# Kernel optimization log

Measured on AMD Instinct MI355X. Metric: run time of the kernel, lower is better.

Reference implementation:

```python
import jax, jax.numpy as jnp
import numpy as np

BN_EPS = 1e-5
K = 3  # k_size


def _unfold(x, k):
    # torch F.unfold with padding=k//2, stride=1, viewed as (B, C, k*k, H, W).
    # Kernel positions are row-major (i slow, j fast), matching torch layout.
    p = k // 2
    B, C, H, W = x.shape
    xp = jnp.pad(x, ((0, 0), (0, 0), (p, p), (p, p)))
    pats = jnp.stack([xp[:, :, i:i + H, j:j + W]
                      for i in range(k) for j in range(k)], axis=2)
    return pats  # (B, C, k*k, H, W)


def _conv1x1(x, w, b):
    # w: (C_out, C_in), x: (B, C_in, H, W)
    return jnp.einsum('oc,bchw->bohw', w, x) + b[None, :, None, None]


def _bn(x, gamma, beta, mean, var):
    inv = gamma / jnp.sqrt(var + BN_EPS)
    return x * inv[None, :, None, None] + (beta - mean * inv)[None, :, None, None]


def setup_inputs() -> dict:
    key = jax.random.key(0)
    ks = jax.random.split(key, 12)
    B, C, H, W = 8, 256, 64, 64
    s = lambda k_, *sh: jax.random.normal(k_, sh, dtype=jnp.float32) * 0.05
    return {
        'x': jax.random.normal(ks[0], (B, C, H, W), dtype=jnp.float32),
        # feature_embedding: Conv2d(C, C, 1) + BN
        'w_embed': s(ks[1], C, C), 'b_embed': jnp.zeros((C,), jnp.float32),
        'bn1_gamma': jnp.ones((C,), jnp.float32), 'bn1_beta': jnp.zeros((C,), jnp.float32),
        'bn1_mean': jnp.zeros((C,), jnp.float32), 'bn1_var': jnp.ones((C,), jnp.float32),
        # enhance: Conv2d(2C, C, 1) + BN
        'w_enh': s(ks[2], C, 2 * C), 'b_enh': jnp.zeros((C,), jnp.float32),
        'bn2_gamma': jnp.ones((C,), jnp.float32), 'bn2_beta': jnp.zeros((C,), jnp.float32),
        'bn2_mean': jnp.zeros((C,), jnp.float32), 'bn2_var': jnp.ones((C,), jnp.float32),
        # weight_gen: Conv2d(2C, C//4, 1) -> ReLU -> Conv2d(C//4, C, 1) -> Sigmoid
        'w_g1': s(ks[3], C // 4, 2 * C), 'b_g1': jnp.zeros((C // 4,), jnp.float32),
        'w_g2': s(ks[4], C, C // 4), 'b_g2': jnp.zeros((C,), jnp.float32),
    }


def reference(x, w_embed, b_embed, bn1_gamma, bn1_beta, bn1_mean, bn1_var,
              w_enh, b_enh, bn2_gamma, bn2_beta, bn2_mean, bn2_var,
              w_g1, b_g1, w_g2, b_g2):
    B, C, H, W = x.shape
    # ---- feature embedding: 1x1 conv + BN (eval) + ReLU
    fe = jax.nn.relu(_bn(_conv1x1(x, w_embed, b_embed),
                         bn1_gamma, bn1_beta, bn1_mean, bn1_var))
    # ---- region similarity: cosine(center pixel, each kxk neighbor) over C
    pats = _unfold(fe, K)                       # (B, C, k2, H, W)
    sim = jnp.einsum('bchw,bckhw->bkhw', fe, pats)
    norm_c = jnp.sqrt(jnp.sum(fe * fe, axis=1))             # (B, H, W)
    norm_p = jnp.sqrt(jnp.sum(pats * pats, axis=1))         # (B, k2, H, W)
    sim = sim / (norm_c[:, None] * norm_p + 1e-7)
    sim = jax.nn.softmax(sim, axis=1)                       # over k2 window
    # ---- dynamic feature aggregation on original x
    xpats = _unfold(x, K)                                   # (B, C, k2, H, W)
    agg = jnp.einsum('bckhw,bkhw->bchw', xpats, sim)
    enhanced = jax.nn.relu(_bn(_conv1x1(jnp.concatenate([x, agg], axis=1), w_enh, b_enh),
                               bn2_gamma, bn2_beta, bn2_mean, bn2_var))
    # ---- output modulation (SE-style gating)
    pooled = jnp.mean(jnp.concatenate([x, enhanced], axis=1), axis=(2, 3), keepdims=True)
    h = jax.nn.relu(_conv1x1(pooled, w_g1, b_g1))
    weights = jax.nn.sigmoid(_conv1x1(h, w_g2, b_g2))       # (B, C, 1, 1)
    return x + weights * enhanced
```

## Files before the change

kernel.cpp:

```cpp
#include <hip/hip_runtime.h>
#include <math.h>

typedef unsigned short u16;
typedef unsigned int   u32;
typedef __attribute__((ext_vector_type(8))) short short8;
typedef __attribute__((ext_vector_type(4))) float f32x4;

#define HW 4096

#define OFS_XB   0ul
#define OFS_PD   8388608ul
#define OFS_W1B  8683520ul
#define OFS_W2B  8716288ul
#define OFS_B1   8781824ul
#define OFS_B2   8782080ul
#define OFS_POOL 8782336ul
#define OFS_GATE 8786432ul
#define OFS_ENH  8788480ul

__device__ __forceinline__ u16 f2bf(float x) {
    union { float f; u32 u; } v; v.f = x;
    u32 r = v.u + 0x7fffu + ((v.u >> 16) & 1u);
    return (u16)(r >> 16);
}
__device__ __forceinline__ float bf2f(u16 h) {
    union { u32 u; float f; } v; v.u = ((u32)h) << 16;
    return v.f;
}
__device__ __forceinline__ void ld_g2l_16(u16* l, const u16* g) {
    __builtin_amdgcn_global_load_lds(
        (const __attribute__((address_space(1))) u32*)g,
        (__attribute__((address_space(3))) u32*)l,
        16, 0, 0);
}

__global__ __launch_bounds__(256) void k_cvt(
    const float* __restrict__ x, u16* __restrict__ xb, float* __restrict__ pool,
    const float* __restrict__ w1, const float* __restrict__ b1,
    const float* __restrict__ g1, const float* __restrict__ be1,
    const float* __restrict__ m1, const float* __restrict__ v1,
    const float* __restrict__ w2, const float* __restrict__ b2,
    const float* __restrict__ g2, const float* __restrict__ be2,
    const float* __restrict__ m2, const float* __restrict__ v2,
    u16* __restrict__ w1b, u16* __restrict__ w2b,
    float* __restrict__ b1f, float* __restrict__ b2f,
    float* __restrict__ pd)
{
    __shared__ float tile[64][65];
    const int t = threadIdx.x;
    const int id = blockIdx.x;
    if (id >= 2048) {
        const int pidb = id - 2048;
        if (pidb >= 770) {
            const int zid = pidb - 770;
            const float4 z = {0.f, 0.f, 0.f, 0.f};
            if (zid < 288) ((float4*)(pd + zid * 1024))[t] = z;
            else           ((float4*)(pool + (zid - 288) * 1024))[t] = z;
            return;
        }
        int idx = pidb * 256 + t;
        if (idx < 65536) {
            int o = idx >> 8;
            float inv = g1[o] * rsqrtf(v1[o] + 1e-5f);
            w1b[idx] = f2bf(w1[idx] * inv);
        } else if (idx < 196608) {
            int j = idx - 65536;
            int o = j >> 9;
            float inv = g2[o] * rsqrtf(v2[o] + 1e-5f);
            w2b[j] = f2bf(w2[j] * inv);
        } else if (idx < 196864) {
            int o = idx - 196608;
            float inv = g1[o] * rsqrtf(v1[o] + 1e-5f);
            b1f[o] = b1[o] * inv + be1[o] - m1[o] * inv;
        } else if (idx < 197120) {
            int o = idx - 196864;
            float inv = g2[o] * rsqrtf(v2[o] + 1e-5f);
            b2f[o] = b2[o] * inv + be2[o] - m2[o] * inv;
        }
        return;
    }
    const int pt = id & 63, ct = (id >> 6) & 3, b = id >> 8;
    const float* src = x + (((size_t)(b * 256 + ct * 64)) << 12) + pt * 64;
#pragma unroll
    for (int i = 0; i < 16; ++i) {
        int idx = i * 256 + t;
        int cl = idx >> 6, pl = idx & 63;
        tile[cl][pl] = src[((size_t)cl << 12) + pl];
    }
    __syncthreads();
#pragma unroll
    for (int i = 0; i < 8; ++i) {
        int idx = i * 256 + t;
        int pl = idx >> 5, c2 = idx & 31;
        int cl = c2 * 2;
        u32 lo = f2bf(tile[cl][pl]);
        u32 hi = f2bf(tile[cl + 1][pl]);
        u32 pv = lo | (hi << 16);
        *(u32*)(xb + (((size_t)(b * 4096 + pt * 64 + pl)) << 9) + ct * 64 + cl) = pv;
    }
    if (t < 64) {
        float s = 0.f;
#pragma unroll
        for (int i = 0; i < 64; ++i) s += tile[t][i];
        atomicAdd(&pool[(b << 9) + ct * 64 + t], s * (1.f / 4096.f));
    }
}

template<int KIN, bool OUTBF, bool DOPOOL>
__global__ __launch_bounds__(256) void k_gemm(
    const u16* __restrict__ xb, const u16* __restrict__ Wb,
    const float* __restrict__ biasf, void* __restrict__ outp,
    float* __restrict__ poolp)
{
    __shared__ __align__(16) u16 Wl[4096];
    __shared__ __align__(16) u16 Xl[4096];
    __shared__ float sbias[128];
    const int t = threadIdx.x;
    const int lane = t & 63;
    const int wv = t >> 6;
    const int p_blk = blockIdx.y * 128;
    const int o_blk = blockIdx.x * 128;
    const int owg = (wv & 1) * 4;
    const int pwg = (wv >> 1) * 4;
    const int r16 = lane & 15, q = lane >> 4;
    if (t < 128) sbias[t] = biasf[o_blk + t];

    f32x4 acc[4][4];
#pragma unroll
    for (int i = 0; i < 4; ++i)
#pragma unroll
        for (int j = 0; j < 4; ++j) acc[i][j] = (f32x4){0.f, 0.f, 0.f, 0.f};

    for (int kc = 0; kc < KIN / 32; ++kc) {
        const int kk = kc * 32 + q * 8;
#pragma unroll
        for (int s = 0; s < 4; ++s) {
            const int bi = wv * 4 + s;
            const u16* g;
            u16* l;
            if (bi < 8) {
                g = Wb + (size_t)(o_blk + bi * 16 + r16) * KIN + kk;
                l = Wl + bi * 512;
            } else {
                g = xb + (((size_t)(p_blk + (bi - 8) * 16 + r16)) << 9) + kk;
                l = Xl + (bi - 8) * 512;
            }
            ld_g2l_16(l, g);
        }
        __syncthreads();
        short8 af[4], bf[4];
#pragma unroll
        for (int i = 0; i < 4; ++i) af[i] = *(const short8*)(Wl + (owg + i) * 512 + lane * 8);
#pragma unroll
        for (int j = 0; j < 4; ++j) bf[j] = *(const short8*)(Xl + (pwg + j) * 512 + lane * 8);
#pragma unroll
        for (int i = 0; i < 4; ++i)
#pragma unroll
            for (int j = 0; j < 4; ++j)
                acc[i][j] = __builtin_amdgcn_mfma_f32_16x16x32_bf16(af[i], bf[j], acc[i][j], 0, 0, 0);
        __syncthreads();
    }

    float bia[4][4];
#pragma unroll
    for (int i = 0; i < 4; ++i)
#pragma unroll
        for (int r = 0; r < 4; ++r) bia[i][r] = sbias[owg * 16 + i * 16 + q * 4 + r];
    const int bidx = p_blk >> 12;
    const int pin0 = (p_blk & 4095) + pwg * 16 + r16;
#pragma unroll
    for (int i = 0; i < 4; ++i) {
#pragma unroll
        for (int r = 0; r < 4; ++r) {
            const int o = o_blk + owg * 16 + i * 16 + q * 4 + r;
            const size_t rowb = ((size_t)(bidx * 256 + o)) << 12;
            float ps = 0.f;
#pragma unroll
            for (int j = 0; j < 4; ++j) {
                float v = fmaxf(acc[i][j][r] + bia[i][r], 0.f);
                const size_t oi = rowb + pin0 + j * 16;
                if (OUTBF) ((u16*)outp)[oi] = f2bf(v);
                else       ((float*)outp)[oi] = v;
                ps += v;
            }
            if (DOPOOL) {
                ps += __shfl_down(ps, 8, 16);
                ps += __shfl_down(ps, 4, 16);
                ps += __shfl_down(ps, 2, 16);
                ps += __shfl_down(ps, 1, 16);
                if (r16 == 0)
                    atomicAdd(&poolp[(bidx << 9) + 256 + o], ps * (1.f / 4096.f));
            }
        }
    }
}

__global__ __launch_bounds__(256) void k_sim(
    const u16* __restrict__ fe, float* __restrict__ pd)
{
    __shared__ __align__(16) u16 st[3 * 4096];
    __shared__ float red[4][64][9];
    const int t = threadIdx.x;
    const int id = blockIdx.x;
    const int g = id & 3, h = (id >> 2) & 63, b = id >> 8;
    const int rows[3] = {h > 0 ? h - 1 : 0, h, h < 63 ? h + 1 : 63};
    const u16* base = fe + (((size_t)(b * 256 + g * 64)) << 12);
#pragma unroll
    for (int it = 0; it < 6; ++it) {
        const int flat = it * 256 + t;
        const int r = flat >> 9, j = flat & 511;
        const u16* gs = base + ((size_t)(j >> 3) << 12) + rows[r] * 64 + (j & 7) * 8;
        ld_g2l_16(st + r * 4096 + j * 8, gs);
    }
    __syncthreads();
    const int w = t & 63, sl = t >> 6;
    const int wl = w > 0 ? w - 1 : 0, wr = w < 63 ? w + 1 : 63;
    float dot[9] = {};
    const u16* s0 = st + sl * 16 * 64;
#pragma unroll 4
    for (int ci = 0; ci < 16; ++ci) {
        const u16* pc = s0 + ci * 64;
        float v[9];
#pragma unroll
        for (int r = 0; r < 3; ++r) {
            v[r * 3 + 0] = bf2f(pc[r * 4096 + wl]);
            v[r * 3 + 1] = bf2f(pc[r * 4096 + w]);
            v[r * 3 + 2] = bf2f(pc[r * 4096 + wr]);
        }
        const float c0 = v[4];
#pragma unroll
        for (int k = 0; k < 9; ++k) dot[k] = fmaf(c0, v[k], dot[k]);
    }
#pragma unroll
    for (int k = 0; k < 9; ++k) red[sl][w][k] = dot[k];
    __syncthreads();
    if (t < 64) {
        const int p = h * 64 + w;
#pragma unroll
        for (int k = 0; k < 9; ++k) {
            float s = red[0][w][k] + red[1][w][k] + red[2][w][k] + red[3][w][k];
            atomicAdd(&pd[((size_t)(b * 9 + k) << 12) + p], s);
        }
    }
}

__global__ __launch_bounds__(256) void k_agg(
    const u16* __restrict__ xb, const float* __restrict__ pd,
    u16* __restrict__ xbo)
{
    __shared__ __align__(16) u16 xt[3 * 4096];
    __shared__ float ws9[9][64];
    const int t = threadIdx.x;
    const int id = blockIdx.x;
    const int g = id & 3, h = (id >> 2) & 63, b = id >> 8;
    const int rows[3] = {h > 0 ? h - 1 : 0, h, h < 63 ? h + 1 : 63};
    const u16* base = xb + (((size_t)(b * 4096)) << 9) + g * 64;
#pragma unroll
    for (int it = 0; it < 6; ++it) {
        const int flat = it * 256 + t;
        const int r = flat >> 9, j = flat & 511;
        const u16* gs = base + (((size_t)(rows[r] * 64 + (j >> 3))) << 9) + (j & 7) * 8;
        ld_g2l_16(xt + r * 4096 + j * 8, gs);
    }
    if (t < 64) {
        const int w = t;
        const int p = h * 64 + w;
        const float* pb = pd + (((size_t)(b * 9)) << 12);
        const float nc = sqrtf(pb[(4 << 12) + p]);
        float s[9], mk[9];
#pragma unroll
        for (int di = -1; di <= 1; ++di)
#pragma unroll
            for (int dj = -1; dj <= 1; ++dj) {
                const int k = (di + 1) * 3 + (dj + 1);
                const int hn = h + di, wn = w + dj;
                const float mask = (hn >= 0 && hn < 64 && wn >= 0 && wn < 64) ? 1.f : 0.f;
                const int hc = hn < 0 ? 0 : (hn > 63 ? 63 : hn);
                const int wc = wn < 0 ? 0 : (wn > 63 ? 63 : wn);
                const float nk = pb[(4 << 12) + hc * 64 + wc];
                const float dk = pb[(k << 12) + p];
                mk[k] = mask;
                s[k] = mask * dk / (nc * sqrtf(nk) + 1e-7f);
            }
        float mx = s[0];
#pragma unroll
        for (int k = 1; k < 9; ++k) mx = fmaxf(mx, s[k]);
        float e[9], sum = 0.f;
#pragma unroll
        for (int k = 0; k < 9; ++k) { e[k] = expf(s[k] - mx); sum += e[k]; }
        const float rs = 1.f / sum;
#pragma unroll
        for (int k = 0; k < 9; ++k) ws9[k][w] = mk[k] * e[k] * rs;
    }
    __syncthreads();
    const int c = t & 63, pg = t >> 6;
    u16* orow = xbo + (((size_t)(b * 4096 + h * 64)) << 9) + 256 + g * 64 + c;
#pragma unroll 4
    for (int pi = 0; pi < 16; ++pi) {
        const int px = pg * 16 + pi;
        const int pl = px > 0 ? px - 1 : 0, pr = px < 63 ? px + 1 : 63;
        const int pxs[3] = {pl, px, pr};
        float m[9];
#pragma unroll
        for (int k = 0; k < 9; ++k) m[k] = ws9[k][px];
        float acc = 0.f;
#pragma unroll
        for (int r = 0; r < 3; ++r)
#pragma unroll
            for (int j = 0; j < 3; ++j)
                acc = fmaf(bf2f(xt[r * 4096 + pxs[j] * 64 + c]), m[r * 3 + j], acc);
        orow[(size_t)px << 9] = f2bf(acc);
    }
}

__global__ __launch_bounds__(64) void k_mlp(
    const float* __restrict__ pool,
    const float* __restrict__ wg1, const float* __restrict__ bg1,
    const float* __restrict__ wg2, const float* __restrict__ bg2,
    float* __restrict__ gate)
{
    __shared__ float pl[512];
    __shared__ float hb[64];
    const int b = blockIdx.x, t = threadIdx.x;
    for (int i = t; i < 512; i += 64) pl[i] = pool[b * 512 + i];
    __syncthreads();
    float s = bg1[t];
    const float* wr = wg1 + t * 512;
    for (int c = 0; c < 512; ++c) s = fmaf(wr[c], pl[c], s);
    hb[t] = fmaxf(s, 0.f);
    __syncthreads();
#pragma unroll
    for (int rr = 0; rr < 4; ++rr) {
        const int o = t + rr * 64;
        float s2 = bg2[o];
        const float* w2 = wg2 + o * 64;
        for (int j = 0; j < 64; ++j) s2 = fmaf(w2[j], hb[j], s2);
        gate[b * 256 + o] = 1.f / (1.f + expf(-s2));
    }
}

__global__ __launch_bounds__(256) void k_final(
    const u16* __restrict__ xb, const u16* __restrict__ enh,
    const float* __restrict__ gate, float* __restrict__ out)
{
    const int t = threadIdx.x;
    const int id = blockIdx.x;
    const int b = id >> 6, rg = id & 63;
    const int w = t & 63, s = t >> 6;
    const int p = rg * 64 + w;
    const u16* xrow = xb + (((size_t)(b * 4096 + p)) << 9) + s * 64;
#pragma unroll 2
    for (int cc = 0; cc < 8; ++cc) {
        short8 xv = *(const short8*)(xrow + cc * 8);
#pragma unroll
        for (int u = 0; u < 8; ++u) {
            const int c = s * 64 + cc * 8 + u;
            const float gt = gate[(b << 8) + c];
            const size_t off = (((size_t)(b * 256 + c)) << 12) + p;
            out[off] = fmaf(gt, bf2f(enh[off]), bf2f((u16)xv[u]));
        }
    }
}

extern "C" void kernel_launch(void* const* d_in, const int* in_sizes, int n_in,
                              void* d_out, int out_size, void* d_ws, size_t ws_size,
                              hipStream_t stream)
{
    const float* x       = (const float*)d_in[0];
    const float* w_embed = (const float*)d_in[1];
    const float* b_embed = (const float*)d_in[2];
    const float* g1      = (const float*)d_in[3];
    const float* be1     = (const float*)d_in[4];
    const float* m1      = (const float*)d_in[5];
    const float* v1      = (const float*)d_in[6];
    const float* w_enh   = (const float*)d_in[7];
    const float* b_enh   = (const float*)d_in[8];
    const float* g2      = (const float*)d_in[9];
    const float* be2     = (const float*)d_in[10];
    const float* m2      = (const float*)d_in[11];
    const float* v2      = (const float*)d_in[12];
    const float* w_g1    = (const float*)d_in[13];
    const float* b_g1    = (const float*)d_in[14];
    const float* w_g2    = (const float*)d_in[15];
    const float* b_g2    = (const float*)d_in[16];
    float* ws  = (float*)d_ws;
    float* out = (float*)d_out;

    u16*   xb   = (u16*)(ws + OFS_XB);
    float* pd   = ws + OFS_PD;
    u16*   w1b  = (u16*)(ws + OFS_W1B);
    u16*   w2b  = (u16*)(ws + OFS_W2B);
    float* b1f  = ws + OFS_B1;
    float* b2f  = ws + OFS_B2;
    float* pool = ws + OFS_POOL;
    float* gate = ws + OFS_GATE;
    u16*   enh  = (u16*)(ws + OFS_ENH);
    u16*   fe   = (u16*)d_out;

    k_cvt<<<dim3(3110), dim3(256), 0, stream>>>(
        x, xb, pool,
        w_embed, b_embed, g1, be1, m1, v1,
        w_enh, b_enh, g2, be2, m2, v2, w1b, w2b, b1f, b2f, pd);
    k_gemm<256, true, false><<<dim3(2, 256), dim3(256), 0, stream>>>(xb, w1b, b1f, (void*)fe, nullptr);
    k_sim<<<dim3(2048), dim3(256), 0, stream>>>(fe, pd);
    k_agg<<<dim3(2048), dim3(256), 0, stream>>>(xb, pd, xb);
    k_gemm<512, true, true><<<dim3(2, 256), dim3(256), 0, stream>>>(xb, w2b, b2f, (void*)enh, pool);
    k_mlp<<<dim3(8), dim3(64), 0, stream>>>(pool, w_g1, b_g1, w_g2, b_g2, gate);
    k_final<<<dim3(512), dim3(256), 0, stream>>>(xb, enh, gate, out);
}
```

Before: 215.1 us.

## Fuse similarity and aggregation kernels using pixel-major fe layout

Merges the separate similarity kernel and aggregation kernel into one k_simagg kernel. The embedding GEMM now writes fe in pixel-major (channel-contiguous) layout so each block loads a 3x34 pixel halo with all 256 channels. Norms, dot products and softmax weights are computed in shared memory, which removes the global pd buffer, its zeroing, and the atomics. The trade-offs are scattered 2-byte stores from the first GEMM in the transposed layout, and heavier shuffle reductions per pixel.

```diff
diff --git a/kernel.cpp b/kernel.cpp
--- a/kernel.cpp
+++ b/kernel.cpp
@@ -9,7 +9,6 @@
 #define HW 4096
 
 #define OFS_XB   0ul
-#define OFS_PD   8388608ul
 #define OFS_W1B  8683520ul
 #define OFS_W2B  8716288ul
 #define OFS_B1   8781824ul
@@ -43,22 +42,18 @@
     const float* __restrict__ g2, const float* __restrict__ be2,
     const float* __restrict__ m2, const float* __restrict__ v2,
     u16* __restrict__ w1b, u16* __restrict__ w2b,
-    float* __restrict__ b1f, float* __restrict__ b2f,
-    float* __restrict__ pd)
+    float* __restrict__ b1f, float* __restrict__ b2f)
 {
     __shared__ float tile[64][65];
     const int t = threadIdx.x;
     const int id = blockIdx.x;
-    if (id >= 2048) {
-        const int pidb = id - 2048;
-        if (pidb >= 770) {
-            const int zid = pidb - 770;
-            const float4 z = {0.f, 0.f, 0.f, 0.f};
-            if (zid < 288) ((float4*)(pd + zid * 1024))[t] = z;
-            else           ((float4*)(pool + (zid - 288) * 1024))[t] = z;
-            return;
-        }
-        int idx = pidb * 256 + t;
+    if (id < 4) {
+        const float4 z = {0.f, 0.f, 0.f, 0.f};
+        ((float4*)(pool + id * 1024))[t] = z;
+        return;
+    }
+    if (id < 774) {
+        int idx = (id - 4) * 256 + t;
         if (idx < 65536) {
             int o = idx >> 8;
             float inv = g1[o] * rsqrtf(v1[o] + 1e-5f);
@@ -79,7 +74,8 @@
         }
         return;
     }
-    const int pt = id & 63, ct = (id >> 6) & 3, b = id >> 8;
+    const int cid = id - 774;
+    const int pt = cid & 63, ct = (cid >> 6) & 3, b = cid >> 8;
     const float* src = x + (((size_t)(b * 256 + ct * 64)) << 12) + pt * 64;
 #pragma unroll
     for (int i = 0; i < 16; ++i) {
@@ -95,8 +91,7 @@
         int cl = c2 * 2;
         u32 lo = f2bf(tile[cl][pl]);
         u32 hi = f2bf(tile[cl + 1][pl]);
-        u32 pv = lo | (hi << 16);
-        *(u32*)(xb + (((size_t)(b * 4096 + pt * 64 + pl)) << 9) + ct * 64 + cl) = pv;
+        *(u32*)(xb + (((size_t)(b * 4096 + pt * 64 + pl)) << 9) + ct * 64 + cl) = lo | (hi << 16);
     }
     if (t < 64) {
         float s = 0.f;
@@ -106,7 +101,7 @@
     }
 }
 
-template<int KIN, bool OUTBF, bool DOPOOL>
+template<int KIN, int MODE>
 __global__ __launch_bounds__(256) void k_gemm(
     const u16* __restrict__ xb, const u16* __restrict__ Wb,
     const float* __restrict__ biasf, void* __restrict__ outp,
@@ -173,17 +168,20 @@
 #pragma unroll
         for (int r = 0; r < 4; ++r) {
             const int o = o_blk + owg * 16 + i * 16 + q * 4 + r;
-            const size_t rowb = ((size_t)(bidx * 256 + o)) << 12;
             float ps = 0.f;
 #pragma unroll
             for (int j = 0; j < 4; ++j) {
                 float v = fmaxf(acc[i][j][r] + bia[i][r], 0.f);
-                const size_t oi = rowb + pin0 + j * 16;
-                if (OUTBF) ((u16*)outp)[oi] = f2bf(v);
-                else       ((float*)outp)[oi] = v;
+                if (MODE == 0) {
+                    const size_t p = (size_t)(p_blk + pwg * 16 + r16 + j * 16);
+                    ((u16*)outp)[(p << 8) + o] = f2bf(v);
+                } else {
+                    const size_t oi = (((size_t)(bidx * 256 + o)) << 12) + pin0 + j * 16;
+                    ((u16*)outp)[oi] = f2bf(v);
+                }
                 ps += v;
             }
-            if (DOPOOL) {
+            if (MODE == 1) {
                 ps += __shfl_down(ps, 8, 16);
                 ps += __shfl_down(ps, 4, 16);
                 ps += __shfl_down(ps, 2, 16);
@@ -195,92 +193,108 @@
     }
 }
 
-__global__ __launch_bounds__(256) void k_sim(
-    const u16* __restrict__ fe, float* __restrict__ pd)
-{
-    __shared__ __align__(16) u16 st[3 * 4096];
-    __shared__ float red[4][64][9];
+__global__ __launch_bounds__(256) void k_simagg(
+    const u16* __restrict__ feT, const u16* __restrict__ xb, u16* __restrict__ xbo)
+{
+    __shared__ __align__(16) u16 st[104 * 256];
+    __shared__ float nsq[102];
+    __shared__ float dot9[32][9];
+    __shared__ float ws9[9][32];
     const int t = threadIdx.x;
     const int id = blockIdx.x;
-    const int g = id & 3, h = (id >> 2) & 63, b = id >> 8;
+    const int half = id & 1, h = (id >> 1) & 63, b = id >> 7;
+    const int w0 = half * 32;
     const int rows[3] = {h > 0 ? h - 1 : 0, h, h < 63 ? h + 1 : 63};
-    const u16* base = fe + (((size_t)(b * 256 + g * 64)) << 12);
-#pragma unroll
-    for (int it = 0; it < 6; ++it) {
-        const int flat = it * 256 + t;
-        const int r = flat >> 9, j = flat & 511;
-        const u16* gs = base + ((size_t)(j >> 3) << 12) + rows[r] * 64 + (j & 7) * 8;
-        ld_g2l_16(st + r * 4096 + j * 8, gs);
-    }
-    __syncthreads();
-    const int w = t & 63, sl = t >> 6;
-    const int wl = w > 0 ? w - 1 : 0, wr = w < 63 ? w + 1 : 63;
-    float dot[9] = {};
-    const u16* s0 = st + sl * 16 * 64;
-#pragma unroll 4
-    for (int ci = 0; ci < 16; ++ci) {
-        const u16* pc = s0 + ci * 64;
-        float v[9];
-#pragma unroll
-        for (int r = 0; r < 3; ++r) {
-            v[r * 3 + 0] = bf2f(pc[r * 4096 + wl]);
-            v[r * 3 + 1] = bf2f(pc[r * 4096 + w]);
-            v[r * 3 + 2] = bf2f(pc[r * 4096 + wr]);
+    const size_t pbase = (size_t)b * 4096;
+
+#pragma unroll
+    for (int it = 0; it < 13; ++it) {
+        const int u = it * 256 + t;
+        int pos = u >> 5; if (pos > 101) pos = 101;
+        const int chunk = u & 31;
+        const int r = pos / 34, wloc = pos - r * 34;
+        int wg = w0 - 1 + wloc; wg = wg < 0 ? 0 : (wg > 63 ? 63 : wg);
+        ld_g2l_16(st + u * 8, feT + ((pbase + rows[r] * 64 + wg) << 8) + chunk * 8);
+    }
+    __syncthreads();
+
+#pragma unroll 2
+    for (int it = 0; it < 13; ++it) {
+        const int u = it * 256 + t;
+        int pos = u >> 5; const int cs = u & 31;
+        const bool valid = pos <= 101; if (!valid) pos = 101;
+        const short8 v = *(const short8*)(st + pos * 256 + cs * 8);
+        float s = 0.f;
+#pragma unroll
+        for (int e = 0; e < 8; ++e) { const float f = bf2f((u16)v[e]); s = fmaf(f, f, s); }
+        s += __shfl_xor(s, 1, 64);
+        s += __shfl_xor(s, 2, 64);
+        s += __shfl_xor(s, 4, 64);
+        s += __shfl_xor(s, 8, 64);
+        s += __shfl_xor(s, 16, 64);
+        if (cs == 0 && valid) nsq[pos] = s;
+    }
+
+    {
+        const int lane = t & 63, wave = t >> 6;
+        const int cs = lane & 31, wq = lane >> 5;
+        const int c8 = cs * 8;
+#pragma unroll
+        for (int pi = 0; pi < 4; ++pi) {
+            const int px = (wave * 2 + wq) * 4 + pi;
+            const short8 cv = *(const short8*)(st + (34 + px + 1) * 256 + c8);
+            float cf[8];
+#pragma unroll
+            for (int e = 0; e < 8; ++e) cf[e] = bf2f((u16)cv[e]);
+            float d[9];
+#pragma unroll
+            for (int dr = 0; dr < 3; ++dr)
+#pragma unroll
+                for (int dj = 0; dj < 3; ++dj) {
+                    const short8 nv = *(const short8*)(st + (dr * 34 + px + dj) * 256 + c8);
+                    float a = 0.f;
+#pragma unroll
+                    for (int e = 0; e < 8; ++e) a = fmaf(cf[e], bf2f((u16)nv[e]), a);
+                    d[dr * 3 + dj] = a;
+                }
+#pragma unroll
+            for (int k = 0; k < 9; ++k) {
+                float a = d[k];
+                a += __shfl_xor(a, 1, 64);
+                a += __shfl_xor(a, 2, 64);
+                a += __shfl_xor(a, 4, 64);
+                a += __shfl_xor(a, 8, 64);
+                a += __shfl_xor(a, 16, 64);
+                if (cs == 0) dot9[px][k] = a;
+            }
         }
-        const float c0 = v[4];
-#pragma unroll
-        for (int k = 0; k < 9; ++k) dot[k] = fmaf(c0, v[k], dot[k]);
-    }
-#pragma unroll
-    for (int k = 0; k < 9; ++k) red[sl][w][k] = dot[k];
-    __syncthreads();
-    if (t < 64) {
-        const int p = h * 64 + w;
-#pragma unroll
-        for (int k = 0; k < 9; ++k) {
-            float s = red[0][w][k] + red[1][w][k] + red[2][w][k] + red[3][w][k];
-            atomicAdd(&pd[((size_t)(b * 9 + k) << 12) + p], s);
-        }
-    }
-}
-
-__global__ __launch_bounds__(256) void k_agg(
-    const u16* __restrict__ xb, const float* __restrict__ pd,
-    u16* __restrict__ xbo)
-{
-    __shared__ __align__(16) u16 xt[3 * 4096];
-    __shared__ float ws9[9][64];
-    const int t = threadIdx.x;
-    const int id = blockIdx.x;
-    const int g = id & 3, h = (id >> 2) & 63, b = id >> 8;
-    const int rows[3] = {h > 0 ? h - 1 : 0, h, h < 63 ? h + 1 : 63};
-    const u16* base = xb + (((size_t)(b * 4096)) << 9) + g * 64;
-#pragma unroll
-    for (int it = 0; it < 6; ++it) {
-        const int flat = it * 256 + t;
-        const int r = flat >> 9, j = flat & 511;
-        const u16* gs = base + (((size_t)(rows[r] * 64 + (j >> 3))) << 9) + (j & 7) * 8;
-        ld_g2l_16(xt + r * 4096 + j * 8, gs);
-    }
-    if (t < 64) {
-        const int w = t;
-        const int p = h * 64 + w;
-        const float* pb = pd + (((size_t)(b * 9)) << 12);
-        const float nc = sqrtf(pb[(4 << 12) + p]);
+    }
+    __syncthreads();
+
+#pragma unroll
+    for (int it = 0; it < 13; ++it) {
+        const int u = it * 256 + t;
+        int pos = u >> 5; if (pos > 101) pos = 101;
+        const int chunk = u & 31;
+        const int r = pos / 34, wloc = pos - r * 34;
+        int wg = w0 - 1 + wloc; wg = wg < 0 ? 0 : (wg > 63 ? 63 : wg);
+        ld_g2l_16(st + u * 8, xb + ((pbase + rows[r] * 64 + wg) << 9) + chunk * 8);
+    }
+    if (t < 32) {
+        const int px = t;
+        const int wgl = w0 + px;
+        const float nc = sqrtf(nsq[34 + px + 1]);
         float s[9], mk[9];
 #pragma unroll
         for (int di = -1; di <= 1; ++di)
 #pragma unroll
             for (int dj = -1; dj <= 1; ++dj) {
                 const int k = (di + 1) * 3 + (dj + 1);
-                const int hn = h + di, wn = w + dj;
+                const int hn = h + di, wn = wgl + dj;
                 const float mask = (hn >= 0 && hn < 64 && wn >= 0 && wn < 64) ? 1.f : 0.f;
-                const int hc = hn < 0 ? 0 : (hn > 63 ? 63 : hn);
-                const int wc = wn < 0 ? 0 : (wn > 63 ? 63 : wn);
-                const float nk = pb[(4 << 12) + hc * 64 + wc];
-                const float dk = pb[(k << 12) + p];
+                const float nk = nsq[(di + 1) * 34 + px + 1 + dj];
                 mk[k] = mask;
-                s[k] = mask * dk / (nc * sqrtf(nk) + 1e-7f);
+                s[k] = mask * dot9[px][k] / (nc * sqrtf(nk) + 1e-7f);
             }
         float mx = s[0];
 #pragma unroll
@@ -290,26 +304,28 @@
         for (int k = 0; k < 9; ++k) { e[k] = expf(s[k] - mx); sum += e[k]; }
         const float rs = 1.f / sum;
 #pragma unroll
-        for (int k = 0; k < 9; ++k) ws9[k][w] = mk[k] * e[k] * rs;
-    }
-    __syncthreads();
-    const int c = t & 63, pg = t >> 6;
-    u16* orow = xbo + (((size_t)(b * 4096 + h * 64)) << 9) + 256 + g * 64 + c;
-#pragma unroll 4
-    for (int pi = 0; pi < 16; ++pi) {
-        const int px = pg * 16 + pi;
-        const int pl = px > 0 ? px - 1 : 0, pr = px < 63 ? px + 1 : 63;
-        const int pxs[3] = {pl, px, pr};
-        float m[9];
-#pragma unroll
-        for (int k = 0; k < 9; ++k) m[k] = ws9[k][px];
-        float acc = 0.f;
-#pragma unroll
-        for (int r = 0; r < 3; ++r)
-#pragma unroll
-            for (int j = 0; j < 3; ++j)
-                acc = fmaf(bf2f(xt[r * 4096 + pxs[j] * 64 + c]), m[r * 3 + j], acc);
-        orow[(size_t)px << 9] = f2bf(acc);
+        for (int k = 0; k < 9; ++k) ws9[k][px] = mk[k] * e[k] * rs;
+    }
+    __syncthreads();
+
+#pragma unroll
+    for (int it = 0; it < 4; ++it) {
+        const int u = it * 256 + t;
+        const int cs = u & 31, px = u >> 5;
+        float acc[8] = {};
+#pragma unroll
+        for (int dr = 0; dr < 3; ++dr)
+#pragma unroll
+            for (int dj = 0; dj < 3; ++dj) {
+                const float wk = ws9[dr * 3 + dj][px];
+                const short8 nv = *(const short8*)(st + (dr * 34 + px + dj) * 256 + cs * 8);
+#pragma unroll
+                for (int e = 0; e < 8; ++e) acc[e] = fmaf(bf2f((u16)nv[e]), wk, acc[e]);
+            }
+        union { u16 a[8]; short8 v; } pk;
+#pragma unroll
+        for (int e = 0; e < 8; ++e) pk.a[e] = f2bf(acc[e]);
+        *(short8*)(xbo + ((pbase + h * 64 + w0 + px) << 9) + 256 + cs * 8) = pk.v;
     }
 }
 
@@ -387,7 +403,6 @@
     float* out = (float*)d_out;
 
     u16*   xb   = (u16*)(ws + OFS_XB);
-    float* pd   = ws + OFS_PD;
     u16*   w1b  = (u16*)(ws + OFS_W1B);
     u16*   w2b  = (u16*)(ws + OFS_W2B);
     float* b1f  = ws + OFS_B1;
@@ -395,16 +410,15 @@
     float* pool = ws + OFS_POOL;
     float* gate = ws + OFS_GATE;
     u16*   enh  = (u16*)(ws + OFS_ENH);
-    u16*   fe   = (u16*)d_out;
-
-    k_cvt<<<dim3(3110), dim3(256), 0, stream>>>(
+    u16*   feT  = (u16*)d_out;
+
+    k_cvt<<<dim3(2822), dim3(256), 0, stream>>>(
         x, xb, pool,
         w_embed, b_embed, g1, be1, m1, v1,
-        w_enh, b_enh, g2, be2, m2, v2, w1b, w2b, b1f, b2f, pd);
-    k_gemm<256, true, false><<<dim3(2, 256), dim3(256), 0, stream>>>(xb, w1b, b1f, (void*)fe, nullptr);
-    k_sim<<<dim3(2048), dim3(256), 0, stream>>>(fe, pd);
-    k_agg<<<dim3(2048), dim3(256), 0, stream>>>(xb, pd, xb);
-    k_gemm<512, true, true><<<dim3(2, 256), dim3(256), 0, stream>>>(xb, w2b, b2f, (void*)enh, pool);
+        w_enh, b_enh, g2, be2, m2, v2, w1b, w2b, b1f, b2f);
+    k_gemm<256, 0><<<dim3(2, 256), dim3(256), 0, stream>>>(xb, w1b, b1f, (void*)feT, nullptr);
+    k_simagg<<<dim3(1024), dim3(256), 0, stream>>>(feT, xb, xb);
+    k_gemm<512, 1><<<dim3(2, 256), dim3(256), 0, stream>>>(xb, w2b, b2f, (void*)enh, pool);
     k_mlp<<<dim3(8), dim3(64), 0, stream>>>(pool, w_g1, b_g1, w_g2, b_g2, gate);
     k_final<<<dim3(512), dim3(256), 0, stream>>>(xb, enh, gate, out);
 }
```

Result: slower. 225.0 us (+4.6%).
